# Kernel tuning notes

Measured on AMD Instinct MI355X. Metric: run time of the kernel, lower is better.

## Reference

```python
import jax, jax.numpy as jnp
import numpy as np

D = 2048
N = 65536


def setup_inputs() -> dict:
    key = jax.random.key(0)
    k1, k2, k3, k4, k5 = jax.random.split(key, 5)
    return {
        "embed_word_l": jax.random.normal(k1, (1, D), dtype=jnp.float32),
        "embed_word_r": jax.random.normal(k2, (1, D), dtype=jnp.float32),
        "embed_candidates_l": jax.random.normal(k3, (N, D), dtype=jnp.float32),
        "embed_candidates_r": jax.random.normal(k4, (N, D), dtype=jnp.float32),
        "W_a": jax.random.truncated_normal(k5, -2.0, 2.0, (D, D), dtype=jnp.float32) * 0.5,
        "b_a": jnp.zeros((1, D), dtype=jnp.float32),
    }


def _determine_attention(embed_word, embed_opposite_candidates, W_a, b_a):
    # embed_word: [1, D]; embed_opposite_candidates: [N, D]
    align = jnp.tanh(embed_word @ W_a + b_a)                 # [1, D]
    scores = embed_opposite_candidates @ align.T             # [N, 1]
    attn = jax.nn.softmax(scores, axis=0)                    # softmax over candidates
    return jnp.sum(attn * embed_opposite_candidates, axis=0, keepdims=True)  # [1, D]


def reference(embed_word_l, embed_word_r, embed_candidates_l, embed_candidates_r, W_a, b_a):
    embed_aggre_word_l = _determine_attention(embed_word_l, embed_candidates_r, W_a, b_a)
    embed_aggre_word_r = _determine_attention(embed_word_r, embed_candidates_l, W_a, b_a)
    return (embed_aggre_word_l, embed_aggre_word_r)
```

## Files before the change

### kernel.cpp

```cpp
#include <hip/hip_runtime.h>
#include <math.h>

#define DDIM 2048
#define NCAND 65536
#define KSPLIT 32

__global__ void align_partial(const float* __restrict__ wl,
                              const float* __restrict__ wr,
                              const float* __restrict__ W,
                              float* __restrict__ alignp) {
    const int j  = blockIdx.x * blockDim.x + threadIdx.x;
    const int kc = blockIdx.y;
    const int kchunk = DDIM / KSPLIT;
    const int k0 = kc * kchunk;
    float al = 0.f, ar = 0.f;
    for (int k = k0; k < k0 + kchunk; ++k) {
        float w = W[(size_t)k * DDIM + j];
        al = fmaf(wl[k], w, al);
        ar = fmaf(wr[k], w, ar);
    }
    alignp[(size_t)(0 * KSPLIT + kc) * DDIM + j] = al;
    alignp[(size_t)(1 * KSPLIT + kc) * DDIM + j] = ar;
}

__global__ void align_finish(const float* __restrict__ alignp,
                             const float* __restrict__ b,
                             float* __restrict__ alignv) {
    const int j = blockIdx.x * blockDim.x + threadIdx.x;
    float sl = b[j], sr = b[j];
    for (int kc = 0; kc < KSPLIT; ++kc) {
        sl += alignp[(size_t)(0 * KSPLIT + kc) * DDIM + j];
        sr += alignp[(size_t)(1 * KSPLIT + kc) * DDIM + j];
    }
    alignv[j] = tanhf(sl);
    alignv[DDIM + j] = tanhf(sr);
}

__global__ __launch_bounds__(256, 4) void score_accum(
    const float* __restrict__ cand_l, const float* __restrict__ cand_r,
    const float* __restrict__ alignv,
    float* __restrict__ accP, float* __restrict__ mP, float* __restrict__ sP,
    int B, int rows_per_wave)
{
    const int side = blockIdx.y;
    const float* __restrict__ cand  = (side == 0) ? cand_r : cand_l;
    const float* __restrict__ align = alignv + (size_t)side * DDIM;

    const int t = threadIdx.x;
    const int w = t >> 6;
    const int l = t & 63;
    const int cbase = l * 4;

    float4 al[8], acc[8];
#pragma unroll
    for (int c = 0; c < 8; ++c) {
        al[c]  = *(const float4*)(align + c * 256 + cbase);
        acc[c] = make_float4(0.f, 0.f, 0.f, 0.f);
    }
    float m = -INFINITY, s = 0.f;

    const int row0 = (blockIdx.x * 4 + w) * rows_per_wave;
    for (int r = 0; r < rows_per_wave; ++r) {
        const float* rp = cand + (size_t)(row0 + r) * DDIM;
        float4 v[8];
#pragma unroll
        for (int c = 0; c < 8; ++c)
            v[c] = *(const float4*)(rp + c * 256 + cbase);
        float p = 0.f;
#pragma unroll
        for (int c = 0; c < 8; ++c) {
            p = fmaf(v[c].x, al[c].x, p);
            p = fmaf(v[c].y, al[c].y, p);
            p = fmaf(v[c].z, al[c].z, p);
            p = fmaf(v[c].w, al[c].w, p);
        }
#pragma unroll
        for (int off = 32; off > 0; off >>= 1)
            p += __shfl_xor(p, off, 64);
        p = __shfl(p, 0, 64);

        if (p > m) {
            float alpha = expf(m - p);
            m = p;
            s = fmaf(s, alpha, 1.f);
#pragma unroll
            for (int c = 0; c < 8; ++c) {
                acc[c].x = fmaf(acc[c].x, alpha, v[c].x);
                acc[c].y = fmaf(acc[c].y, alpha, v[c].y);
                acc[c].z = fmaf(acc[c].z, alpha, v[c].z);
                acc[c].w = fmaf(acc[c].w, alpha, v[c].w);
            }
        } else {
            float wgt = expf(p - m);
            s += wgt;
#pragma unroll
            for (int c = 0; c < 8; ++c) {
                acc[c].x = fmaf(wgt, v[c].x, acc[c].x);
                acc[c].y = fmaf(wgt, v[c].y, acc[c].y);
                acc[c].z = fmaf(wgt, v[c].z, acc[c].z);
                acc[c].w = fmaf(wgt, v[c].w, acc[c].w);
            }
        }
    }

    __shared__ float sh_acc[4][DDIM];
    __shared__ float sh_m[4], sh_s[4];
#pragma unroll
    for (int c = 0; c < 8; ++c)
        *(float4*)(&sh_acc[w][c * 256 + cbase]) = acc[c];
    if (l == 0) { sh_m[w] = m; sh_s[w] = s; }
    __syncthreads();

    const float mB = fmaxf(fmaxf(sh_m[0], sh_m[1]), fmaxf(sh_m[2], sh_m[3]));
    const float e0 = expf(sh_m[0] - mB);
    const float e1 = expf(sh_m[1] - mB);
    const float e2 = expf(sh_m[2] - mB);
    const float e3 = expf(sh_m[3] - mB);
    const float sB = e0 * sh_s[0] + e1 * sh_s[1] + e2 * sh_s[2] + e3 * sh_s[3];

    float* accB = accP + (size_t)(side * B + blockIdx.x) * DDIM;
#pragma unroll
    for (int half = 0; half < 2; ++half) {
        const int col = half * 1024 + t * 4;
        const float4 a0 = *(const float4*)&sh_acc[0][col];
        const float4 a1 = *(const float4*)&sh_acc[1][col];
        const float4 a2 = *(const float4*)&sh_acc[2][col];
        const float4 a3 = *(const float4*)&sh_acc[3][col];
        float4 o;
        o.x = e0 * a0.x + e1 * a1.x + e2 * a2.x + e3 * a3.x;
        o.y = e0 * a0.y + e1 * a1.y + e2 * a2.y + e3 * a3.y;
        o.z = e0 * a0.z + e1 * a1.z + e2 * a2.z + e3 * a3.z;
        o.w = e0 * a0.w + e1 * a1.w + e2 * a2.w + e3 * a3.w;
        *(float4*)(accB + col) = o;
    }
    if (t == 0) {
        mP[side * B + blockIdx.x] = mB;
        sP[side * B + blockIdx.x] = sB;
    }
}

__global__ void combine(const float* __restrict__ accP,
                        const float* __restrict__ mP,
                        const float* __restrict__ sP,
                        float* __restrict__ out, int B)
{
    const int side = blockIdx.y;
    const int j = blockIdx.x * blockDim.x + threadIdx.x;
    const float* m = mP + side * B;
    const float* s = sP + side * B;
    float M = -INFINITY;
    for (int b = 0; b < B; ++b) M = fmaxf(M, m[b]);
    float S = 0.f, num = 0.f;
    for (int b = 0; b < B; ++b) {
        float w = expf(m[b] - M);
        S += w * s[b];
        num = fmaf(w, accP[(size_t)(side * B + b) * DDIM + j], num);
    }
    out[(size_t)side * DDIM + j] = num / S;
}

extern "C" void kernel_launch(void* const* d_in, const int* in_sizes, int n_in,
                              void* d_out, int out_size, void* d_ws, size_t ws_size,
                              hipStream_t stream) {
    const float* wl = (const float*)d_in[0];
    const float* wr = (const float*)d_in[1];
    const float* cl = (const float*)d_in[2];
    const float* cr = (const float*)d_in[3];
    const float* W  = (const float*)d_in[4];
    const float* ba = (const float*)d_in[5];
    float* out = (float*)d_out;
    float* ws  = (float*)d_ws;

    const size_t fixed_f = (size_t)2 * KSPLIT * DDIM + (size_t)2 * DDIM;
    int B = 512;
    while (B > 8) {
        size_t need = (fixed_f + (size_t)4 * B + (size_t)2 * B * DDIM) * sizeof(float);
        if (need <= ws_size) break;
        B >>= 1;
    }
    const int rpw = NCAND / (B * 4);

    float* alignp = ws;
    float* alignv = alignp + (size_t)2 * KSPLIT * DDIM;
    float* mP     = alignv + (size_t)2 * DDIM;
    float* sP     = mP + (size_t)2 * B;
    float* accP   = sP + (size_t)2 * B;

    align_partial<<<dim3(DDIM / 256, KSPLIT), 256, 0, stream>>>(wl, wr, W, alignp);
    align_finish<<<dim3(DDIM / 256), 256, 0, stream>>>(alignp, ba, alignv);
    score_accum<<<dim3(B, 2), 256, 0, stream>>>(cl, cr, alignv, accP, mP, sP, B, rpw);
    combine<<<dim3(DDIM / 256, 2), 256, 0, stream>>>(accP, mP, sP, out, B);
}
```

Baseline: 1.161 ms.

## Vectorize align GEMV, split dot-product chains, skip negligible softmax rows, unroll combine

The align_partial kernel now makes float4 loads of W with a quarter of the blocks. The score dot product uses four independent accumulators and drops the redundant lane broadcast after the xor-reduction. Rows whose score is more than 25 below the running max are skipped in the accumulation. The combine kernel is unrolled by four with independent accumulators. The row skip slightly changes numerics, and it assumes B is a multiple of 4.

Result: faster. 1.074 ms (-7.5%).

```diff
diff --git a/kernel.cpp b/kernel.cpp
--- a/kernel.cpp
+++ b/kernel.cpp
@@ -9,18 +9,22 @@
                               const float* __restrict__ wr,
                               const float* __restrict__ W,
                               float* __restrict__ alignp) {
-    const int j  = blockIdx.x * blockDim.x + threadIdx.x;
+    const int j4 = blockIdx.x * blockDim.x + threadIdx.x;
     const int kc = blockIdx.y;
     const int kchunk = DDIM / KSPLIT;
     const int k0 = kc * kchunk;
-    float al = 0.f, ar = 0.f;
+    float4 al = make_float4(0.f, 0.f, 0.f, 0.f);
+    float4 ar = make_float4(0.f, 0.f, 0.f, 0.f);
     for (int k = k0; k < k0 + kchunk; ++k) {
-        float w = W[(size_t)k * DDIM + j];
-        al = fmaf(wl[k], w, al);
-        ar = fmaf(wr[k], w, ar);
-    }
-    alignp[(size_t)(0 * KSPLIT + kc) * DDIM + j] = al;
-    alignp[(size_t)(1 * KSPLIT + kc) * DDIM + j] = ar;
+        const float4 w = *(const float4*)(W + (size_t)k * DDIM + j4 * 4);
+        const float cl = wl[k], cr = wr[k];
+        al.x = fmaf(cl, w.x, al.x); al.y = fmaf(cl, w.y, al.y);
+        al.z = fmaf(cl, w.z, al.z); al.w = fmaf(cl, w.w, al.w);
+        ar.x = fmaf(cr, w.x, ar.x); ar.y = fmaf(cr, w.y, ar.y);
+        ar.z = fmaf(cr, w.z, ar.z); ar.w = fmaf(cr, w.w, ar.w);
+    }
+    *(float4*)(alignp + (size_t)(0 * KSPLIT + kc) * DDIM + j4 * 4) = al;
+    *(float4*)(alignp + (size_t)(1 * KSPLIT + kc) * DDIM + j4 * 4) = ar;
 }
 
 __global__ void align_finish(const float* __restrict__ alignp,
@@ -66,21 +70,24 @@
 #pragma unroll
         for (int c = 0; c < 8; ++c)
             v[c] = *(const float4*)(rp + c * 256 + cbase);
-        float p = 0.f;
+
+        float pp[4] = {0.f, 0.f, 0.f, 0.f};
 #pragma unroll
         for (int c = 0; c < 8; ++c) {
-            p = fmaf(v[c].x, al[c].x, p);
-            p = fmaf(v[c].y, al[c].y, p);
-            p = fmaf(v[c].z, al[c].z, p);
-            p = fmaf(v[c].w, al[c].w, p);
+            float q = pp[c >> 1];
+            q = fmaf(v[c].x, al[c].x, q);
+            q = fmaf(v[c].y, al[c].y, q);
+            q = fmaf(v[c].z, al[c].z, q);
+            q = fmaf(v[c].w, al[c].w, q);
+            pp[c >> 1] = q;
         }
+        float p = (pp[0] + pp[1]) + (pp[2] + pp[3]);
 #pragma unroll
         for (int off = 32; off > 0; off >>= 1)
             p += __shfl_xor(p, off, 64);
-        p = __shfl(p, 0, 64);
 
         if (p > m) {
-            float alpha = expf(m - p);
+            const float alpha = expf(m - p);
             m = p;
             s = fmaf(s, alpha, 1.f);
 #pragma unroll
@@ -90,8 +97,8 @@
                 acc[c].z = fmaf(acc[c].z, alpha, v[c].z);
                 acc[c].w = fmaf(acc[c].w, alpha, v[c].w);
             }
-        } else {
-            float wgt = expf(p - m);
+        } else if (p - m >= -25.f) {
+            const float wgt = expf(p - m);
             s += wgt;
 #pragma unroll
             for (int c = 0; c < 8; ++c) {
@@ -148,15 +155,32 @@
     const int j = blockIdx.x * blockDim.x + threadIdx.x;
     const float* m = mP + side * B;
     const float* s = sP + side * B;
-    float M = -INFINITY;
-    for (int b = 0; b < B; ++b) M = fmaxf(M, m[b]);
-    float S = 0.f, num = 0.f;
-    for (int b = 0; b < B; ++b) {
-        float w = expf(m[b] - M);
-        S += w * s[b];
-        num = fmaf(w, accP[(size_t)(side * B + b) * DDIM + j], num);
-    }
-    out[(size_t)side * DDIM + j] = num / S;
+    float M0 = -INFINITY, M1 = -INFINITY, M2 = -INFINITY, M3 = -INFINITY;
+    for (int b = 0; b < B; b += 4) {
+        M0 = fmaxf(M0, m[b]);
+        M1 = fmaxf(M1, m[b + 1]);
+        M2 = fmaxf(M2, m[b + 2]);
+        M3 = fmaxf(M3, m[b + 3]);
+    }
+    const float M = fmaxf(fmaxf(M0, M1), fmaxf(M2, M3));
+
+    float S0 = 0.f, S1 = 0.f, S2 = 0.f, S3 = 0.f;
+    float n0 = 0.f, n1 = 0.f, n2 = 0.f, n3 = 0.f;
+    const float* ap = accP + (size_t)side * B * DDIM + j;
+    for (int b = 0; b < B; b += 4) {
+        const float w0 = expf(m[b]     - M);
+        const float w1 = expf(m[b + 1] - M);
+        const float w2 = expf(m[b + 2] - M);
+        const float w3 = expf(m[b + 3] - M);
+        S0 += w0 * s[b];     S1 += w1 * s[b + 1];
+        S2 += w2 * s[b + 2]; S3 += w3 * s[b + 3];
+        n0 = fmaf(w0, ap[(size_t)(b)     * DDIM], n0);
+        n1 = fmaf(w1, ap[(size_t)(b + 1) * DDIM], n1);
+        n2 = fmaf(w2, ap[(size_t)(b + 2) * DDIM], n2);
+        n3 = fmaf(w3, ap[(size_t)(b + 3) * DDIM], n3);
+    }
+    out[(size_t)side * DDIM + j] =
+        ((n0 + n1) + (n2 + n3)) / ((S0 + S1) + (S2 + S3));
 }
 
 extern "C" void kernel_launch(void* const* d_in, const int* in_sizes, int n_in,
@@ -186,7 +210,7 @@
     float* sP     = mP + (size_t)2 * B;
     float* accP   = sP + (size_t)2 * B;
 
-    align_partial<<<dim3(DDIM / 256, KSPLIT), 256, 0, stream>>>(wl, wr, W, alignp);
+    align_partial<<<dim3(DDIM / 1024, KSPLIT), 256, 0, stream>>>(wl, wr, W, alignp);
     align_finish<<<dim3(DDIM / 256), 256, 0, stream>>>(alignp, ba, alignv);
     score_accum<<<dim3(B, 2), 256, 0, stream>>>(cl, cr, alignv, accP, mP, sP, B, rpw);
     combine<<<dim3(DDIM / 256, 2), 256, 0, stream>>>(accP, mP, sP, out, B);
```
